# Performance work log

Hardware: AMD Instinct MI355X
Metric: run time of the kernel (lower is better)

## Reference

```python
import jax, jax.numpy as jnp
import numpy as np

OUT_SL = 32


def gru_cell(x, h, Wih, Whh, bih, bhh):
    # PyTorch GRU cell: gates ordered (r, z, n)
    gi = x @ Wih.T + bih
    gh = h @ Whh.T + bhh
    ir, iz, inn = jnp.split(gi, 3, axis=-1)
    hr, hz, hn = jnp.split(gh, 3, axis=-1)
    r = jax.nn.sigmoid(ir + hr)
    z = jax.nn.sigmoid(iz + hz)
    n = jnp.tanh(inn + r * hn)
    return (1.0 - z) * n + z * h


def run_gru_layer(xs, h0, Wih, Whh, bih, bhh, reverse=False):
    def step(h, x):
        h = gru_cell(x, h, Wih, Whh, bih, bhh)
        return h, h
    hT, ys = jax.lax.scan(step, h0, xs, reverse=reverse)
    return ys, hT


def setup_inputs() -> dict:
    key = jax.random.key(0)
    ks = iter(jax.random.split(key, 32))

    def p(shape, fan_in):
        return (jax.random.normal(next(ks), shape, dtype=jnp.float32)
                / np.sqrt(fan_in).astype(np.float32))

    V_ENC, V_DEC, EE, ED, NH = 32000, 32000, 300, 300, 256
    inp = jax.random.randint(next(ks), (128, 64), 0, V_ENC)
    return {
        'emb_enc': p((V_ENC, EE), 1.0),
        'enc_Wih0': p((2, 3 * NH, EE), EE),
        'enc_Whh0': p((2, 3 * NH, NH), NH),
        'enc_bih0': p((2, 3 * NH), NH),
        'enc_bhh0': p((2, 3 * NH), NH),
        'enc_Wih1': p((2, 3 * NH, 2 * NH), 2 * NH),
        'enc_Whh1': p((2, 3 * NH, NH), NH),
        'enc_bih1': p((2, 3 * NH), NH),
        'enc_bhh1': p((2, 3 * NH), NH),
        'W_out_enc': p((ED, 2 * NH), 2 * NH),
        'emb_dec': p((V_DEC, ED), 1.0),
        'dec_Wih': p((2, 3 * ED, ED), ED),
        'dec_Whh': p((2, 3 * ED, ED), ED),
        'dec_bih': p((2, 3 * ED), ED),
        'dec_bhh': p((2, 3 * ED), ED),
        'W1': p((2 * NH, ED), 2 * NH),
        'l2_W': p((ED, ED), ED),
        'l2_b': p((ED,), ED),
        'l3_W': p((ED, ED + 2 * NH), ED + 2 * NH),
        'l3_b': p((ED,), ED),
        'V_att': p((ED,), ED),
        'out_b': p((V_DEC,), ED),
        'inp': inp,
    }


def reference(emb_enc, enc_Wih0, enc_Whh0, enc_bih0, enc_bhh0,
              enc_Wih1, enc_Whh1, enc_bih1, enc_bhh1, W_out_enc,
              emb_dec, dec_Wih, dec_Whh, dec_bih, dec_bhh,
              W1, l2_W, l2_b, l3_W, l3_b, V_att, out_b, inp):
    sl, bs = inp.shape
    nh = enc_Whh0.shape[-1]
    h0 = jnp.zeros((bs, nh), dtype=emb_enc.dtype)

    # ---- encoder: 2-layer bidirectional GRU (dropout in eval mode = identity)
    emb = emb_enc[inp]                                        # (sl, bs, EE)
    yf0, hf0 = run_gru_layer(emb, h0, enc_Wih0[0], enc_Whh0[0], enc_bih0[0], enc_bhh0[0])
    yb0, hb0 = run_gru_layer(emb, h0, enc_Wih0[1], enc_Whh0[1], enc_bih0[1], enc_bhh0[1], reverse=True)
    x1 = jnp.concatenate([yf0, yb0], axis=-1)                 # (sl, bs, 2*nh)
    yf1, hf1 = run_gru_layer(x1, h0, enc_Wih1[0], enc_Whh1[0], enc_bih1[0], enc_bhh1[0])
    yb1, hb1 = run_gru_layer(x1, h0, enc_Wih1[1], enc_Whh1[1], enc_bih1[1], enc_bhh1[1], reverse=True)
    enc_out = jnp.concatenate([yf1, yb1], axis=-1)            # (sl, bs, 2*nh)

    # h.view(2,2,bs,-1).permute(0,2,1,3) -> concat fwd/bwd per layer
    h = jnp.stack([jnp.concatenate([hf0, hb0], axis=-1),
                   jnp.concatenate([hf1, hb1], axis=-1)])     # (2, bs, 2*nh)
    h = h @ W_out_enc.T                                       # (2, bs, ED)

    w1e = enc_out @ W1                                        # (sl, bs, ED)
    dec_inp0 = jnp.zeros((bs,), dtype=jnp.int32)

    def dec_step(carry, _):
        h, dec_inp = carry
        w2h = h[-1] @ l2_W.T + l2_b                           # (bs, ED)
        u = jnp.tanh(w1e + w2h[None])                         # (sl, bs, ED)
        a = jax.nn.softmax(u @ V_att, axis=0)                 # (sl, bs), softmax over seq
        Xa = jnp.einsum('sb,sbd->bd', a, enc_out)             # (bs, 2*nh)
        e = emb_dec[dec_inp]                                  # (bs, ED)
        x = jnp.concatenate([e, Xa], axis=1) @ l3_W.T + l3_b  # (bs, ED)
        h0n = gru_cell(x, h[0], dec_Wih[0], dec_Whh[0], dec_bih[0], dec_bhh[0])
        h1n = gru_cell(h0n, h[1], dec_Wih[1], dec_Whh[1], dec_bih[1], dec_bhh[1])
        outp = h1n @ emb_dec.T + out_b                        # (bs, V_dec), tied weights
        ndec = jnp.argmax(outp, axis=1).astype(jnp.int32)
        return (jnp.stack([h0n, h1n]), ndec), outp

    (_, _), res = jax.lax.scan(dec_step, (h, dec_inp0), None, length=OUT_SL)
    return res                                                # (out_sl, bs, V_dec)
```

## Files before the change

### kernel.cpp

```cpp
#include <hip/hip_runtime.h>
#include <math.h>


typedef unsigned long long ull;
typedef float v2f __attribute__((ext_vector_type(2)));

#define DINL static __device__ __forceinline__

DINL float sigm(float x) { return 1.0f / (1.0f + expf(-x)); }
DINL float dot4f(float4 a, float4 b) { return a.x*b.x + a.y*b.y + a.z*b.z + a.w*b.w; }

DINL ull packmax(float x, int v) {
  unsigned u = __float_as_uint(x);
  u = (u & 0x80000000u) ? ~u : (u | 0x80000000u);
  return ((ull)u << 32) | (unsigned)(~v);
}
DINL ull umax64(ull a, ull b) { return a > b ? a : b; }

DINL float atl(const float* p) {
  unsigned u = __hip_atomic_load((const unsigned*)p, __ATOMIC_RELAXED,
                                 __HIP_MEMORY_SCOPE_AGENT);
  return __uint_as_float(u);
}
DINL void atsf(float* p, float v) {
  __hip_atomic_exchange((unsigned*)p, __float_as_uint(v), __ATOMIC_RELAXED,
                        __HIP_MEMORY_SCOPE_AGENT);
}
DINL ull atl64(const ull* p) {
  return __hip_atomic_load(p, __ATOMIC_RELAXED, __HIP_MEMORY_SCOPE_AGENT);
}
DINL void ats64(ull* p, ull v) {
  __hip_atomic_exchange(p, v, __ATOMIC_RELAXED, __HIP_MEMORY_SCOPE_AGENT);
}

DINL void gbar(unsigned* cnt, unsigned target, int tid) {
  asm volatile("s_waitcnt vmcnt(0)" ::: "memory");
  __syncthreads();
  if (tid == 0) {
    __hip_atomic_fetch_add(cnt, 1u, __ATOMIC_RELAXED, __HIP_MEMORY_SCOPE_AGENT);
    while (__hip_atomic_load(cnt, __ATOMIC_RELAXED, __HIP_MEMORY_SCOPE_AGENT) < target)
      __builtin_amdgcn_s_sleep(4);
  }
  __syncthreads();
}

__global__ __launch_bounds__(256) void k_embed(const float4* __restrict__ E,
                                               const int* __restrict__ inp,
                                               float4* __restrict__ out) {
  int i = blockIdx.x * 256 + threadIdx.x;
  if (i >= 8192 * 75) return;
  int row = i / 75, q = i - row * 75;
  out[i] = E[(size_t)inp[row] * 75 + q];
}

__global__ __launch_bounds__(256) void k_transpose(const float* __restrict__ A,
                                                   float* __restrict__ B, int R, int C) {
  __shared__ float tile[32][33];
  int c0 = blockIdx.x * 32, r0 = blockIdx.y * 32;
  int tx = threadIdx.x & 31, ty = threadIdx.x >> 5;
  for (int i = 0; i < 32; i += 8) {
    int r = r0 + ty + i, c = c0 + tx;
    if (r < R && c < C) tile[ty + i][tx] = A[(size_t)r * C + c];
  }
  __syncthreads();
  for (int i = 0; i < 32; i += 8) {
    int c = c0 + ty + i, r = r0 + tx;
    if (c < C && r < R) B[(size_t)c * R + r] = tile[tx][ty + i];
  }
}

__global__ __launch_bounds__(256) void k_packW(const float* __restrict__ Whh,
                                               float* __restrict__ W2) {
  int i = blockIdx.x * 256 + threadIdx.x;
  if (i >= 196608) return;
  int d = i / 98304, r = i - d * 98304, kp = r / 768, gc = r - kp * 768;
  const float* src = Whh + (size_t)d * 196608 + (size_t)gc * 256 + kp * 2;
  float* dst = W2 + (size_t)i * 2;
  dst[0] = src[0];
  dst[1] = src[1];
}

__global__ __launch_bounds__(256) void k_gemm128(const float* __restrict__ A,
                                                 const float* __restrict__ B,
                                                 const float* __restrict__ bias,
                                                 float* __restrict__ C,
                                                 int N, int M, int K) {
  __shared__ float As[8][132];
  __shared__ float Bs[8][132];
  const int tid = threadIdx.x;
  const int bn = blockIdx.x * 128, bm = blockIdx.y * 128;
  const int tn = (tid >> 4) << 3, tm = (tid & 15) << 3;
  const int r = tid & 127;
  const bool isB = tid >= 128;
  const float* src = isB ? (B + (size_t)(bm + r) * K) : (A + (size_t)(bn + r) * K);
  const bool rowok = isB ? (bm + r < M) : (bn + r < N);
  float acc[8][8] = {};
  for (int k0 = 0; k0 < K; k0 += 8) {
    float v[8];
    if (rowok && k0 + 8 <= K) {
      float4 p0 = *(const float4*)(src + k0);
      float4 p1 = *(const float4*)(src + k0 + 4);
      v[0]=p0.x; v[1]=p0.y; v[2]=p0.z; v[3]=p0.w;
      v[4]=p1.x; v[5]=p1.y; v[6]=p1.z; v[7]=p1.w;
    } else {
#pragma unroll
      for (int j = 0; j < 8; ++j) v[j] = (rowok && k0 + j < K) ? src[k0 + j] : 0.0f;
    }
    float (*dst)[132] = isB ? Bs : As;
#pragma unroll
    for (int j = 0; j < 8; ++j) dst[j][r] = v[j];
    __syncthreads();
#pragma unroll
    for (int kk = 0; kk < 8; ++kk) {
      float a[8], b[8];
      *(float4*)&a[0] = *(const float4*)&As[kk][tn];
      *(float4*)&a[4] = *(const float4*)&As[kk][tn + 4];
      *(float4*)&b[0] = *(const float4*)&Bs[kk][tm];
      *(float4*)&b[4] = *(const float4*)&Bs[kk][tm + 4];
#pragma unroll
      for (int i = 0; i < 8; ++i)
#pragma unroll
        for (int j = 0; j < 8; ++j) acc[i][j] += a[i] * b[j];
    }
    __syncthreads();
  }
#pragma unroll
  for (int i = 0; i < 8; ++i) {
    int row = bn + tn + i;
    if (row >= N) continue;
#pragma unroll
    for (int j = 0; j < 8; ++j) {
      int col = bm + tm + j;
      if (col < M) C[(size_t)row * M + col] = acc[i][j] + (bias ? bias[col] : 0.0f);
    }
  }
}

__global__ __launch_bounds__(256) void k_enc_rec(
    const float* __restrict__ giF, const float* __restrict__ giB,
    const float* __restrict__ W2, const float* __restrict__ bhh,
    float* __restrict__ y) {
  const int b0 = blockIdx.x * 2;
  const int dir = blockIdx.y;
  const int c = threadIdx.x;
  const float* gi = dir ? giB : giF;
  const v2f* Wv = (const v2f*)(W2 + (size_t)dir * 196608);
  const float* bh = bhh + dir * 768;

  __shared__ __align__(16) float hls[2][2][258];
  for (int i = c; i < 2 * 2 * 258; i += 256) ((float*)hls)[i] = 0.0f;
  __syncthreads();

  const float bhr = bh[c], bhz = bh[256 + c], bhn = bh[512 + c];
  const int tt0 = dir ? 127 : 0;
  const float* g0p = gi + (size_t)tt0 * 49152 + (size_t)b0 * 768;
  float g0r = g0p[c], g0z = g0p[256 + c], g0n = g0p[512 + c];
  float g1r = g0p[768 + c], g1z = g0p[1024 + c], g1n = g0p[1280 + c];

  for (int t = 0; t < 128; ++t) {
    const int cu = t & 1;
    float p0r = 0, p0z = 0, p0n = 0, p1r = 0, p1z = 0, p1n = 0;
    if (t < 127) {
      const int tn_ = dir ? 126 - t : t + 1;
      const float* gp = gi + (size_t)tn_ * 49152 + (size_t)b0 * 768;
      p0r = gp[c]; p0z = gp[256 + c]; p0n = gp[512 + c];
      p1r = gp[768 + c]; p1z = gp[1024 + c]; p1n = gp[1280 + c];
    }
    v2f a0r = {0,0}, a0z = {0,0}, a0n = {0,0};
    v2f a1r = {0,0}, a1z = {0,0}, a1n = {0,0};
    const float* h0p = &hls[cu][0][0];
    const float* h1p = &hls[cu][1][0];
#pragma unroll 4
    for (int kp = 0; kp < 128; ++kp) {
      v2f wr = Wv[kp * 768 + c];
      v2f wz = Wv[kp * 768 + 256 + c];
      v2f wn = Wv[kp * 768 + 512 + c];
      v2f h0 = *(const v2f*)&h0p[kp * 2];
      v2f h1 = *(const v2f*)&h1p[kp * 2];
      a0r += h0 * wr; a0z += h0 * wz; a0n += h0 * wn;
      a1r += h1 * wr; a1z += h1 * wz; a1n += h1 * wn;
    }
    float r0 = sigm(g0r + a0r.x + a0r.y + bhr);
    float z0 = sigm(g0z + a0z.x + a0z.y + bhz);
    float n0 = tanhf(g0n + r0 * (a0n.x + a0n.y + bhn));
    float h0new = (1.f - z0) * n0 + z0 * h0p[c];
    float r1 = sigm(g1r + a1r.x + a1r.y + bhr);
    float z1 = sigm(g1z + a1z.x + a1z.y + bhz);
    float n1 = tanhf(g1n + r1 * (a1n.x + a1n.y + bhn));
    float h1new = (1.f - z1) * n1 + z1 * h1p[c];
    hls[cu ^ 1][0][c] = h0new;
    hls[cu ^ 1][1][c] = h1new;
    const int tw = dir ? 127 - t : t;
    float* yp = y + (size_t)tw * 32768 + (size_t)b0 * 512 + dir * 256 + c;
    yp[0] = h0new;
    yp[512] = h1new;
    g0r = p0r; g0z = p0z; g0n = p0n; g1r = p1r; g1z = p1z; g1n = p1n;
    __syncthreads();
  }
}

__global__ __launch_bounds__(256) void k_hcat(const float* __restrict__ x1,
                                              const float* __restrict__ encout,
                                              float* __restrict__ hcat) {
  int i = blockIdx.x * 256 + threadIdx.x;
  int l = i >> 15, r = i & 32767, b = r >> 9, d = r & 511;
  const float* src = l ? encout : x1;
  int ts = (d < 256) ? 127 : 0;
  hcat[i] = src[((size_t)(ts << 6) + b) * 512 + d];
}

DINL void gru_lds(int cch, int bch, int tid,
                  const float* __restrict__ xin, const float* __restrict__ hin,
                  float* __restrict__ hout, float* __restrict__ houtT,
                  const float* Wg, const float* biass, float* scr) {
  float* xs = scr;
  float* hs = scr + 4800;
  const int b0 = bch * 16;
  for (int i = tid; i < 4800; i += 256) {
    int row = i / 300, q = i - row * 300;
    xs[i] = atl(xin + (size_t)(b0 + row) * 300 + q);
    hs[i] = atl(hin + (size_t)(b0 + row) * 300 + q);
  }
  __syncthreads();
  const int cl = tid & 15, bl = tid >> 4;
  const int c = cch * 16 + cl, bq = b0 + bl;
  if (c < 300) {
    float gir = biass[cl],      giz = biass[16 + cl], gin = biass[32 + cl];
    float ghr = biass[48 + cl], ghz = biass[64 + cl], ghn = biass[80 + cl];
    const float4* xr = (const float4*)(xs + bl * 300);
    const float4* hr = (const float4*)(hs + bl * 300);
    const float4* w0 = (const float4*)(Wg + (0 * 16 + cl) * 308);
    const float4* w1 = (const float4*)(Wg + (1 * 16 + cl) * 308);
    const float4* w2 = (const float4*)(Wg + (2 * 16 + cl) * 308);
    const float4* w3 = (const float4*)(Wg + (3 * 16 + cl) * 308);
    const float4* w4 = (const float4*)(Wg + (4 * 16 + cl) * 308);
    const float4* w5 = (const float4*)(Wg + (5 * 16 + cl) * 308);
    for (int q = 0; q < 75; ++q) {
      float4 xv = xr[q], hv = hr[q];
      gir += dot4f(xv, w0[q]);
      giz += dot4f(xv, w1[q]);
      gin += dot4f(xv, w2[q]);
      ghr += dot4f(hv, w3[q]);
      ghz += dot4f(hv, w4[q]);
      ghn += dot4f(hv, w5[q]);
    }
    float r = sigm(gir + ghr), z = sigm(giz + ghz);
    float n = tanhf(gin + r * ghn);
    float hnew = (1.f - z) * n + z * hs[bl * 300 + c];
    atsf(&hout[(size_t)bq * 300 + c], hnew);
    if (houtT) atsf(&houtT[(size_t)c * 64 + bq], hnew);
  }
  __syncthreads();
}

__global__ __launch_bounds__(256) void k_dec_all(
    float* __restrict__ dech, float* __restrict__ h1T, float* __restrict__ xdec,
    ull* __restrict__ bests, unsigned* __restrict__ cnt,
    const float* __restrict__ w1e, const float* __restrict__ encout,
    const float* __restrict__ l2W, const float* __restrict__ l2b,
    const float* __restrict__ l3W, const float* __restrict__ l3b,
    const float* __restrict__ Vatt, const float* __restrict__ embdec,
    const float* __restrict__ dWih, const float* __restrict__ dWhh,
    const float* __restrict__ dbih, const float* __restrict__ dbhh,
    const float* __restrict__ embT, const float* __restrict__ outb,
    float* __restrict__ out) {
  const int wg = blockIdx.x, tid = threadIdx.x;
  __shared__ __align__(16) float Wg[6 * 16 * 308];
  __shared__ __align__(16) float scr[9600];
  __shared__ float biass[96];

  int grole = -1, gcell = 0;
  if (wg < 76) { grole = wg; gcell = 0; }
  else if (wg < 152) { grole = wg - 76; gcell = 1; }
  const int cch = (grole >= 0) ? grole % 19 : 0;
  const int bch = (grole >= 0) ? grole / 19 : 0;
  if (grole >= 0) {
    const float* Wih = dWih + gcell * 270000;
    const float* Whh = dWhh + gcell * 270000;
    for (int i = tid; i < 96 * 300; i += 256) {
      int r = i / 300, k = i - r * 300;
      int g = r >> 4, cl = r & 15;
      int c = cch * 16 + cl;
      float v = 0.f;
      if (c < 300)
        v = (g < 3) ? Wih[(size_t)(g * 300 + c) * 300 + k]
                    : Whh[(size_t)((g - 3) * 300 + c) * 300 + k];
      Wg[(g * 16 + cl) * 308 + k] = v;
    }
    if (tid < 96) {
      int g = tid >> 4, cl = tid & 15;
      int c = cch * 16 + cl;
      float v = 0.f;
      if (c < 300)
        v = (g < 3) ? dbih[gcell * 900 + g * 300 + c]
                    : dbhh[gcell * 900 + (g - 3) * 300 + c];
      biass[tid] = v;
    }
  }
  __syncthreads();

  unsigned tgt = 0;
  for (int t = 0; t < 32; ++t) {
    const int cur = t & 1;
    float* hc = dech + cur * 38400;
    float* hn = dech + (cur ^ 1) * 38400;

    if (wg < 64) {
      const int b = wg;
      float* h1s = scr;
      float* w2h = scr + 304;
      float* eXa = scr + 608;
      float* aa  = scr + 1424;
      float* red = scr + 1552;
      ull* redb  = (ull*)(scr + 1680);

      if (tid < 128) {
        ull m = 0ULL;
        if (t > 0) {
          m = atl64(&bests[(size_t)tid * 64 + b]);
          if (tid + 128 < 250) m = umax64(m, atl64(&bests[(size_t)(tid + 128) * 64 + b]));
        }
        redb[tid] = m;
      }
      for (int i = tid; i < 300; i += 256) h1s[i] = atl(hc + 19200 + b * 300 + i);
      __syncthreads();
      for (int s = 64; s > 0; s >>= 1) {
        if (tid < s) redb[tid] = umax64(redb[tid], redb[tid + s]);
        __syncthreads();
      }
      const int ib = (t > 0) ? (int)(~(unsigned)(redb[0] & 0xFFFFFFFFULL)) : 0;

      for (int m = tid; m < 300; m += 256) {
        const float4* wr = (const float4*)(l2W + (size_t)m * 300);
        const float4* hr = (const float4*)h1s;
        float acc = l2b[m];
        for (int q = 0; q < 75; ++q) acc += dot4f(wr[q], hr[q]);
        w2h[m] = acc;
      }
      __syncthreads();

      if (tid < 128) {
        const float4* wp = (const float4*)(w1e + ((size_t)(tid << 6) + b) * 300);
        const float4* vp = (const float4*)Vatt;
        const float4* hp = (const float4*)w2h;
        float acc = 0.f;
        for (int q = 0; q < 75; ++q) {
          float4 w = wp[q], h = hp[q], v = vp[q];
          acc += tanhf(w.x + h.x) * v.x + tanhf(w.y + h.y) * v.y +
                 tanhf(w.z + h.z) * v.z + tanhf(w.w + h.w) * v.w;
        }
        aa[tid] = acc;
        red[tid] = acc;
      }
      __syncthreads();
      for (int s = 64; s > 0; s >>= 1) {
        if (tid < s) red[tid] = fmaxf(red[tid], red[tid + s]);
        __syncthreads();
      }
      float mx = red[0];
      __syncthreads();
      if (tid < 128) {
        float ex = expf(aa[tid] - mx);
        aa[tid] = ex;
        red[tid] = ex;
      }
      __syncthreads();
      for (int s = 64; s > 0; s >>= 1) {
        if (tid < s) red[tid] += red[tid + s];
        __syncthreads();
      }
      float inv = 1.0f / red[0];
      __syncthreads();
      if (tid < 128) aa[tid] *= inv;
      for (int d = tid; d < 300; d += 256) eXa[d] = embdec[(size_t)ib * 300 + d];
      __syncthreads();

      for (int d = tid; d < 512; d += 256) {
        float acc = 0.f;
        for (int s = 0; s < 128; ++s)
          acc += aa[s] * encout[((size_t)(s << 6) + b) * 512 + d];
        eXa[300 + d] = acc;
      }
      __syncthreads();

      for (int m = tid; m < 300; m += 256) {
        const float4* wr = (const float4*)(l3W + (size_t)m * 812);
        const float4* xr = (const float4*)eXa;
        float acc = l3b[m];
        for (int q = 0; q < 203; ++q) acc += dot4f(wr[q], xr[q]);
        atsf(&xdec[b * 300 + m], acc);
      }
      __syncthreads();
    }
    gbar(cnt, 256u * (++tgt), tid);

    if (wg < 76)
      gru_lds(cch, bch, tid, xdec, hc, hn, nullptr, Wg, biass, scr);
    gbar(cnt, 256u * (++tgt), tid);

    if (wg >= 76 && wg < 152)
      gru_lds(cch, bch, tid, hn, hc + 19200, hn + 19200, h1T, Wg, biass, scr);
    gbar(cnt, 256u * (++tgt), tid);

    if (wg < 250) {
      const int v0 = wg * 128;
      const int vq = tid & 31, bo = tid >> 5;
      float acc[8][4];
#pragma unroll
      for (int i = 0; i < 8; ++i)
#pragma unroll
        for (int j = 0; j < 4; ++j) acc[i][j] = 0.f;
      float* hch = scr;
      for (int kc = 0; kc < 4; ++kc) {
        __syncthreads();
        for (int i = tid; i < 4800; i += 256) hch[i] = atl(h1T + kc * 4800 + i);
        __syncthreads();
        const float* eb = embT + (size_t)kc * 75 * 32000 + v0 + (vq << 2);
        for (int k = 0; k < 75; ++k) {
          float4 ev = *(const float4*)(eb + (size_t)k * 32000);
          float hv[8];
          *(float4*)&hv[0] = *(const float4*)&hch[(k << 6) + (bo << 3)];
          *(float4*)&hv[4] = *(const float4*)&hch[(k << 6) + (bo << 3) + 4];
#pragma unroll
          for (int i = 0; i < 8; ++i) {
            acc[i][0] += hv[i] * ev.x;
            acc[i][1] += hv[i] * ev.y;
            acc[i][2] += hv[i] * ev.z;
            acc[i][3] += hv[i] * ev.w;
          }
        }
      }
      float4 bo4 = *(const float4*)(outb + v0 + (vq << 2));
      float* outp = out + (size_t)t * 2048000;
      float* sacc = scr;
      __syncthreads();
#pragma unroll
      for (int i = 0; i < 8; ++i) {
        const int b = (bo << 3) + i;
        float4 r;
        r.x = acc[i][0] + bo4.x; r.y = acc[i][1] + bo4.y;
        r.z = acc[i][2] + bo4.z; r.w = acc[i][3] + bo4.w;
        *(float4*)(outp + (size_t)b * 32000 + v0 + (vq << 2)) = r;
        sacc[((vq << 2) + 0) * 65 + b] = r.x;
        sacc[((vq << 2) + 1) * 65 + b] = r.y;
        sacc[((vq << 2) + 2) * 65 + b] = r.z;
        sacc[((vq << 2) + 3) * 65 + b] = r.w;
      }
      __syncthreads();
      if (tid < 64) {
        ull best = 0ULL;
#pragma unroll 4
        for (int v = 0; v < 128; ++v)
          best = umax64(best, packmax(sacc[v * 65 + tid], v0 + v));
        ats64(&bests[(size_t)wg * 64 + tid], best);
      }
      __syncthreads();
    }
    if (t < 31) gbar(cnt, 256u * (++tgt), tid);
  }
}

extern "C" void kernel_launch(void* const* d_in, const int* in_sizes, int n_in,
                              void* d_out_v, int out_size, void* d_ws, size_t ws_size,
                              hipStream_t stream) {
  (void)in_sizes; (void)n_in; (void)out_size; (void)ws_size;
  const float* emb_enc = (const float*)d_in[0];
  const float* eWih0   = (const float*)d_in[1];
  const float* eWhh0   = (const float*)d_in[2];
  const float* ebih0   = (const float*)d_in[3];
  const float* ebhh0   = (const float*)d_in[4];
  const float* eWih1   = (const float*)d_in[5];
  const float* eWhh1   = (const float*)d_in[6];
  const float* ebih1   = (const float*)d_in[7];
  const float* ebhh1   = (const float*)d_in[8];
  const float* Wout    = (const float*)d_in[9];
  const float* emb_dec = (const float*)d_in[10];
  const float* dWih    = (const float*)d_in[11];
  const float* dWhh    = (const float*)d_in[12];
  const float* dbih    = (const float*)d_in[13];
  const float* dbhh    = (const float*)d_in[14];
  const float* W1      = (const float*)d_in[15];
  const float* l2W     = (const float*)d_in[16];
  const float* l2b     = (const float*)d_in[17];
  const float* l3W     = (const float*)d_in[18];
  const float* l3b     = (const float*)d_in[19];
  const float* Vatt    = (const float*)d_in[20];
  const float* outb    = (const float*)d_in[21];
  const int* inp       = (const int*)d_in[22];
  float* d_out = (float*)d_out_v;

  float* ws = (float*)d_ws;
  size_t off = 0;
  auto take = [&](size_t n) { float* p = ws + off; off += (n + 3) & ~(size_t)3; return p; };
  float* embT   = take((size_t)300 * 32000);
  float* encout = take((size_t)8192 * 512);
  float* w1e    = take((size_t)8192 * 300);
  float* W1T    = take((size_t)300 * 512);
  float* hcat   = take((size_t)128 * 512);
  float* dech   = take((size_t)2 * 2 * 64 * 300);
  float* h1T    = take((size_t)300 * 64);
  float* xdec   = take((size_t)64 * 300);
  ull* bests    = (ull*)take((size_t)250 * 64 * 2);
  unsigned* cnt = (unsigned*)take((size_t)32);

  float* emb  = d_out;
  float* gi0f = emb + 2457600;
  float* gi0b = gi0f + 6291456;
  float* x1   = gi0b + 6291456;
  float* gi1f = x1 + 4194304;
  float* gi1b = gi1f + 6291456;
  float* W2L0 = d_out + 33554432;
  float* W2L1 = W2L0 + 393216;

  hipMemsetAsync(cnt, 0, 32 * sizeof(unsigned), stream);

  k_embed<<<2400, 256, 0, stream>>>((const float4*)emb_enc, inp, (float4*)emb);
  k_transpose<<<dim3(10, 16), 256, 0, stream>>>(W1, W1T, 512, 300);
  k_transpose<<<dim3(10, 1000), 256, 0, stream>>>(emb_dec, embT, 32000, 300);
  k_packW<<<768, 256, 0, stream>>>(eWhh0, W2L0);
  k_packW<<<768, 256, 0, stream>>>(eWhh1, W2L1);

  k_gemm128<<<dim3(64, 6), 256, 0, stream>>>(emb, eWih0, ebih0, gi0f, 8192, 768, 300);
  k_gemm128<<<dim3(64, 6), 256, 0, stream>>>(emb, eWih0 + 230400, ebih0 + 768, gi0b, 8192, 768, 300);
  k_enc_rec<<<dim3(32, 2), 256, 0, stream>>>(gi0f, gi0b, W2L0, ebhh0, x1);

  k_gemm128<<<dim3(64, 6), 256, 0, stream>>>(x1, eWih1, ebih1, gi1f, 8192, 768, 512);
  k_gemm128<<<dim3(64, 6), 256, 0, stream>>>(x1, eWih1 + 393216, ebih1 + 768, gi1b, 8192, 768, 512);
  k_enc_rec<<<dim3(32, 2), 256, 0, stream>>>(gi1f, gi1b, W2L1, ebhh1, encout);

  k_hcat<<<256, 256, 0, stream>>>(x1, encout, hcat);
  k_gemm128<<<dim3(1, 3), 256, 0, stream>>>(hcat, Wout, nullptr, dech, 128, 300, 512);
  k_gemm128<<<dim3(64, 3), 256, 0, stream>>>(encout, W1T, nullptr, w1e, 8192, 300, 512);

  k_dec_all<<<256, 256, 0, stream>>>(dech, h1T, xdec, bests, cnt,
                                     w1e, encout, l2W, l2b, l3W, l3b,
                                     Vatt, emb_dec, dWih, dWhh, dbih, dbhh,
                                     embT, outb, d_out);
}
```

Measured before the change: 10.92 ms.

## Double block size in persistent decoder and stream GRU weights from global

The persistent decoder kernel now runs 512 threads per workgroup. The GRU stage drops its LDS-resident weight slices, reads weights straight from global memory, and splits the K reduction across two thread halves, combining them through shared memory. The output-projection GEMM stages the whole h1T matrix in LDS and double-buffers 32-row chunks of the transposed embedding with register prefetch, so each thread owns a 4x4 tile. The attention stage drops its strided loops because 512 threads cover 300 and 512 outputs directly. This adds parallelism and removes the weight preload, but the GRU weights now travel through L2/global on every step.

Result: slower. 25.51 ms (+133.6%).

```diff
diff --git a/kernel.cpp b/kernel.cpp
--- a/kernel.cpp
+++ b/kernel.cpp
@@ -209,41 +209,59 @@
   hcat[i] = src[((size_t)(ts << 6) + b) * 512 + d];
 }
 
-DINL void gru_lds(int cch, int bch, int tid,
-                  const float* __restrict__ xin, const float* __restrict__ hin,
-                  float* __restrict__ hout, float* __restrict__ houtT,
-                  const float* Wg, const float* biass, float* scr) {
-  float* xs = scr;
-  float* hs = scr + 4800;
+DINL void gru_stream(int cch, int bch, int tid,
+                     const float* __restrict__ xin, const float* __restrict__ hin,
+                     float* __restrict__ hout, float* __restrict__ houtT,
+                     const float* __restrict__ Wih, const float* __restrict__ Whh,
+                     const float* __restrict__ bih, const float* __restrict__ bhh,
+                     float* C) {
+  float* xs = C;
+  float* hs = C + 4800;
+  float* part = C + 9600;
   const int b0 = bch * 16;
-  for (int i = tid; i < 4800; i += 256) {
-    int row = i / 300, q = i - row * 300;
-    xs[i] = atl(xin + (size_t)(b0 + row) * 300 + q);
-    hs[i] = atl(hin + (size_t)(b0 + row) * 300 + q);
-  }
-  __syncthreads();
-  const int cl = tid & 15, bl = tid >> 4;
+  for (int i = tid; i < 9600; i += 512) {
+    int j = (i < 4800) ? i : i - 4800;
+    int row = j / 300, q = j - row * 300;
+    C[i] = atl(((i < 4800) ? xin : hin) + (size_t)(b0 + row) * 300 + q);
+  }
+  __syncthreads();
+  const int cl = tid & 15, bl = (tid >> 4) & 15, ks = tid >> 8;
   const int c = cch * 16 + cl, bq = b0 + bl;
-  if (c < 300) {
-    float gir = biass[cl],      giz = biass[16 + cl], gin = biass[32 + cl];
-    float ghr = biass[48 + cl], ghz = biass[64 + cl], ghn = biass[80 + cl];
+  const bool valid = (c < 300);
+  float a0 = 0, a1 = 0, a2 = 0, a3 = 0, a4 = 0, a5 = 0;
+  if (valid) {
+    const int q0 = ks ? 38 : 0, q1 = ks ? 75 : 38;
     const float4* xr = (const float4*)(xs + bl * 300);
     const float4* hr = (const float4*)(hs + bl * 300);
-    const float4* w0 = (const float4*)(Wg + (0 * 16 + cl) * 308);
-    const float4* w1 = (const float4*)(Wg + (1 * 16 + cl) * 308);
-    const float4* w2 = (const float4*)(Wg + (2 * 16 + cl) * 308);
-    const float4* w3 = (const float4*)(Wg + (3 * 16 + cl) * 308);
-    const float4* w4 = (const float4*)(Wg + (4 * 16 + cl) * 308);
-    const float4* w5 = (const float4*)(Wg + (5 * 16 + cl) * 308);
-    for (int q = 0; q < 75; ++q) {
+    const float4* w0 = (const float4*)(Wih + (size_t)c * 300);
+    const float4* w1 = (const float4*)(Wih + (size_t)(300 + c) * 300);
+    const float4* w2 = (const float4*)(Wih + (size_t)(600 + c) * 300);
+    const float4* w3 = (const float4*)(Whh + (size_t)c * 300);
+    const float4* w4 = (const float4*)(Whh + (size_t)(300 + c) * 300);
+    const float4* w5 = (const float4*)(Whh + (size_t)(600 + c) * 300);
+    for (int q = q0; q < q1; ++q) {
       float4 xv = xr[q], hv = hr[q];
-      gir += dot4f(xv, w0[q]);
-      giz += dot4f(xv, w1[q]);
-      gin += dot4f(xv, w2[q]);
-      ghr += dot4f(hv, w3[q]);
-      ghz += dot4f(hv, w4[q]);
-      ghn += dot4f(hv, w5[q]);
-    }
+      a0 += dot4f(xv, w0[q]);
+      a1 += dot4f(xv, w1[q]);
+      a2 += dot4f(xv, w2[q]);
+      a3 += dot4f(hv, w3[q]);
+      a4 += dot4f(hv, w4[q]);
+      a5 += dot4f(hv, w5[q]);
+    }
+  }
+  const int idx = bl * 16 + cl;
+  if (ks == 1) {
+    part[idx] = a0; part[256 + idx] = a1; part[512 + idx] = a2;
+    part[768 + idx] = a3; part[1024 + idx] = a4; part[1280 + idx] = a5;
+  }
+  __syncthreads();
+  if (ks == 0 && valid) {
+    float gir = a0 + part[idx]        + bih[c];
+    float giz = a1 + part[256 + idx]  + bih[300 + c];
+    float gin = a2 + part[512 + idx]  + bih[600 + c];
+    float ghr = a3 + part[768 + idx]  + bhh[c];
+    float ghz = a4 + part[1024 + idx] + bhh[300 + c];
+    float ghn = a5 + part[1280 + idx] + bhh[600 + c];
     float r = sigm(gir + ghr), z = sigm(giz + ghz);
     float n = tanhf(gin + r * ghn);
     float hnew = (1.f - z) * n + z * hs[bl * 300 + c];
@@ -253,7 +271,7 @@
   __syncthreads();
 }
 
-__global__ __launch_bounds__(256) void k_dec_all(
+__global__ __launch_bounds__(512) void k_dec_all(
     float* __restrict__ dech, float* __restrict__ h1T, float* __restrict__ xdec,
     ull* __restrict__ bests, unsigned* __restrict__ cnt,
     const float* __restrict__ w1e, const float* __restrict__ encout,
@@ -265,54 +283,26 @@
     const float* __restrict__ embT, const float* __restrict__ outb,
     float* __restrict__ out) {
   const int wg = blockIdx.x, tid = threadIdx.x;
-  __shared__ __align__(16) float Wg[6 * 16 * 308];
-  __shared__ __align__(16) float scr[9600];
-  __shared__ float biass[96];
-
-  int grole = -1, gcell = 0;
-  if (wg < 76) { grole = wg; gcell = 0; }
-  else if (wg < 152) { grole = wg - 76; gcell = 1; }
-  const int cch = (grole >= 0) ? grole % 19 : 0;
-  const int bch = (grole >= 0) ? grole / 19 : 0;
-  if (grole >= 0) {
-    const float* Wih = dWih + gcell * 270000;
-    const float* Whh = dWhh + gcell * 270000;
-    for (int i = tid; i < 96 * 300; i += 256) {
-      int r = i / 300, k = i - r * 300;
-      int g = r >> 4, cl = r & 15;
-      int c = cch * 16 + cl;
-      float v = 0.f;
-      if (c < 300)
-        v = (g < 3) ? Wih[(size_t)(g * 300 + c) * 300 + k]
-                    : Whh[(size_t)((g - 3) * 300 + c) * 300 + k];
-      Wg[(g * 16 + cl) * 308 + k] = v;
-    }
-    if (tid < 96) {
-      int g = tid >> 4, cl = tid & 15;
-      int c = cch * 16 + cl;
-      float v = 0.f;
-      if (c < 300)
-        v = (g < 3) ? dbih[gcell * 900 + g * 300 + c]
-                    : dbhh[gcell * 900 + (g - 3) * 300 + c];
-      biass[tid] = v;
-    }
-  }
-  __syncthreads();
+  __shared__ __align__(16) float4 ebuf[2][1024];
+  __shared__ __align__(16) float C[19200];
+
+  const int grole = (wg < 76) ? wg : ((wg < 152) ? wg - 76 : 0);
+  const int cch = grole % 19, bch = grole / 19;
 
   unsigned tgt = 0;
   for (int t = 0; t < 32; ++t) {
-    const int cur = t & 1;
-    float* hc = dech + cur * 38400;
-    float* hn = dech + (cur ^ 1) * 38400;
+    const int cur_ = t & 1;
+    float* hc = dech + cur_ * 38400;
+    float* hn = dech + (cur_ ^ 1) * 38400;
 
     if (wg < 64) {
       const int b = wg;
-      float* h1s = scr;
-      float* w2h = scr + 304;
-      float* eXa = scr + 608;
-      float* aa  = scr + 1424;
-      float* red = scr + 1552;
-      ull* redb  = (ull*)(scr + 1680);
+      float* h1s = C;
+      float* w2h = C + 304;
+      float* eXa = C + 608;
+      float* aa  = C + 1424;
+      float* red = C + 1552;
+      ull* redb  = (ull*)(C + 1680);
 
       if (tid < 128) {
         ull m = 0ULL;
@@ -322,7 +312,7 @@
         }
         redb[tid] = m;
       }
-      for (int i = tid; i < 300; i += 256) h1s[i] = atl(hc + 19200 + b * 300 + i);
+      if (tid < 300) h1s[tid] = atl(hc + 19200 + b * 300 + tid);
       __syncthreads();
       for (int s = 64; s > 0; s >>= 1) {
         if (tid < s) redb[tid] = umax64(redb[tid], redb[tid + s]);
@@ -330,12 +320,12 @@
       }
       const int ib = (t > 0) ? (int)(~(unsigned)(redb[0] & 0xFFFFFFFFULL)) : 0;
 
-      for (int m = tid; m < 300; m += 256) {
-        const float4* wr = (const float4*)(l2W + (size_t)m * 300);
+      if (tid < 300) {
+        const float4* wr = (const float4*)(l2W + (size_t)tid * 300);
         const float4* hr = (const float4*)h1s;
-        float acc = l2b[m];
+        float acc = l2b[tid];
         for (int q = 0; q < 75; ++q) acc += dot4f(wr[q], hr[q]);
-        w2h[m] = acc;
+        w2h[tid] = acc;
       }
       __syncthreads();
 
@@ -372,74 +362,98 @@
       float inv = 1.0f / red[0];
       __syncthreads();
       if (tid < 128) aa[tid] *= inv;
-      for (int d = tid; d < 300; d += 256) eXa[d] = embdec[(size_t)ib * 300 + d];
-      __syncthreads();
-
-      for (int d = tid; d < 512; d += 256) {
+      if (tid < 300) eXa[tid] = embdec[(size_t)ib * 300 + tid];
+      __syncthreads();
+
+      {
+        const float* ebase = encout + (size_t)b * 512 + tid;
         float acc = 0.f;
-        for (int s = 0; s < 128; ++s)
-          acc += aa[s] * encout[((size_t)(s << 6) + b) * 512 + d];
-        eXa[300 + d] = acc;
-      }
-      __syncthreads();
-
-      for (int m = tid; m < 300; m += 256) {
-        const float4* wr = (const float4*)(l3W + (size_t)m * 812);
+        for (int s = 0; s < 128; ++s) acc += aa[s] * ebase[(size_t)s * 32768];
+        eXa[300 + tid] = acc;
+      }
+      __syncthreads();
+
+      if (tid < 300) {
+        const float4* wr = (const float4*)(l3W + (size_t)tid * 812);
         const float4* xr = (const float4*)eXa;
-        float acc = l3b[m];
+        float acc = l3b[tid];
         for (int q = 0; q < 203; ++q) acc += dot4f(wr[q], xr[q]);
-        atsf(&xdec[b * 300 + m], acc);
+        atsf(&xdec[b * 300 + tid], acc);
       }
       __syncthreads();
     }
     gbar(cnt, 256u * (++tgt), tid);
 
     if (wg < 76)
-      gru_lds(cch, bch, tid, xdec, hc, hn, nullptr, Wg, biass, scr);
+      gru_stream(cch, bch, tid, xdec, hc, hn, nullptr,
+                 dWih, dWhh, dbih, dbhh, C);
     gbar(cnt, 256u * (++tgt), tid);
 
     if (wg >= 76 && wg < 152)
-      gru_lds(cch, bch, tid, hn, hc + 19200, hn + 19200, h1T, Wg, biass, scr);
+      gru_stream(cch, bch, tid, hn, hc + 19200, hn + 19200, h1T,
+                 dWih + 270000, dWhh + 270000, dbih + 900, dbhh + 900, C);
     gbar(cnt, 256u * (++tgt), tid);
 
     if (wg < 250) {
       const int v0 = wg * 128;
       const int vq = tid & 31, bo = tid >> 5;
-      float acc[8][4];
-#pragma unroll
-      for (int i = 0; i < 8; ++i)
-#pragma unroll
-        for (int j = 0; j < 4; ++j) acc[i][j] = 0.f;
-      float* hch = scr;
-      for (int kc = 0; kc < 4; ++kc) {
-        __syncthreads();
-        for (int i = tid; i < 4800; i += 256) hch[i] = atl(h1T + kc * 4800 + i);
-        __syncthreads();
-        const float* eb = embT + (size_t)kc * 75 * 32000 + v0 + (vq << 2);
-        for (int k = 0; k < 75; ++k) {
-          float4 ev = *(const float4*)(eb + (size_t)k * 32000);
-          float hv[8];
-          *(float4*)&hv[0] = *(const float4*)&hch[(k << 6) + (bo << 3)];
-          *(float4*)&hv[4] = *(const float4*)&hch[(k << 6) + (bo << 3) + 4];
-#pragma unroll
-          for (int i = 0; i < 8; ++i) {
-            acc[i][0] += hv[i] * ev.x;
-            acc[i][1] += hv[i] * ev.y;
-            acc[i][2] += hv[i] * ev.z;
-            acc[i][3] += hv[i] * ev.w;
+      for (int i = tid; i < 19200; i += 512) C[i] = atl(h1T + i);
+      {
+        const int u0 = tid * 2, u1 = u0 + 1;
+        float4 s0 = *(const float4*)(embT + (size_t)(u0 >> 5) * 32000 + v0 + ((u0 & 31) << 2));
+        float4 s1 = *(const float4*)(embT + (size_t)(u1 >> 5) * 32000 + v0 + ((u1 & 31) << 2));
+        ebuf[0][u0] = s0;
+        ebuf[0][u1] = s1;
+      }
+      __syncthreads();
+
+      float acc[4][4] = {};
+      int cur = 0;
+      for (int kc = 0; kc < 10; ++kc) {
+        const int k0 = kc << 5;
+        const int nrows = (kc < 9) ? 32 : 12;
+        float4 s0, s1;
+        bool h0 = false, h1 = false;
+        if (kc < 9) {
+          const int nk0 = k0 + 32;
+          const int nun = ((kc < 8) ? 32 : 12) << 5;
+          const int u0 = tid * 2, u1 = u0 + 1;
+          if (u0 < nun) {
+            s0 = *(const float4*)(embT + (size_t)(nk0 + (u0 >> 5)) * 32000 + v0 + ((u0 & 31) << 2));
+            h0 = true;
+          }
+          if (u1 < nun) {
+            s1 = *(const float4*)(embT + (size_t)(nk0 + (u1 >> 5)) * 32000 + v0 + ((u1 & 31) << 2));
+            h1 = true;
           }
         }
-      }
-      float4 bo4 = *(const float4*)(outb + v0 + (vq << 2));
+        for (int k = 0; k < nrows; ++k) {
+          float4 ev = ebuf[cur][(k << 5) + vq];
+          float4 hv = *(const float4*)&C[((k0 + k) << 6) + (bo << 2)];
+          acc[0][0] += hv.x * ev.x; acc[0][1] += hv.x * ev.y;
+          acc[0][2] += hv.x * ev.z; acc[0][3] += hv.x * ev.w;
+          acc[1][0] += hv.y * ev.x; acc[1][1] += hv.y * ev.y;
+          acc[1][2] += hv.y * ev.z; acc[1][3] += hv.y * ev.w;
+          acc[2][0] += hv.z * ev.x; acc[2][1] += hv.z * ev.y;
+          acc[2][2] += hv.z * ev.z; acc[2][3] += hv.z * ev.w;
+          acc[3][0] += hv.w * ev.x; acc[3][1] += hv.w * ev.y;
+          acc[3][2] += hv.w * ev.z; acc[3][3] += hv.w * ev.w;
+        }
+        if (h0) ebuf[cur ^ 1][tid * 2] = s0;
+        if (h1) ebuf[cur ^ 1][tid * 2 + 1] = s1;
+        __syncthreads();
+        cur ^= 1;
+      }
+
+      float* sacc = C;
+      float4 ob = *(const float4*)(outb + v0 + (vq << 2));
       float* outp = out + (size_t)t * 2048000;
-      float* sacc = scr;
-      __syncthreads();
-#pragma unroll
-      for (int i = 0; i < 8; ++i) {
-        const int b = (bo << 3) + i;
+#pragma unroll
+      for (int i = 0; i < 4; ++i) {
+        const int b = (bo << 2) + i;
         float4 r;
-        r.x = acc[i][0] + bo4.x; r.y = acc[i][1] + bo4.y;
-        r.z = acc[i][2] + bo4.z; r.w = acc[i][3] + bo4.w;
+        r.x = acc[i][0] + ob.x; r.y = acc[i][1] + ob.y;
+        r.z = acc[i][2] + ob.z; r.w = acc[i][3] + ob.w;
         *(float4*)(outp + (size_t)b * 32000 + v0 + (vq << 2)) = r;
         sacc[((vq << 2) + 0) * 65 + b] = r.x;
         sacc[((vq << 2) + 1) * 65 + b] = r.y;
@@ -532,7 +546,7 @@
   k_gemm128<<<dim3(1, 3), 256, 0, stream>>>(hcat, Wout, nullptr, dech, 128, 300, 512);
   k_gemm128<<<dim3(64, 3), 256, 0, stream>>>(encout, W1T, nullptr, w1e, 8192, 300, 512);
 
-  k_dec_all<<<256, 256, 0, stream>>>(dech, h1T, xdec, bests, cnt,
+  k_dec_all<<<256, 512, 0, stream>>>(dech, h1T, xdec, bests, cnt,
                                      w1e, encout, l2W, l2b, l3W, l3b,
                                      Vatt, emb_dec, dWih, dWhh, dbih, dbhh,
                                      embT, outb, d_out);
```
